# Optimization experiments

Hardware: AMD Instinct MI355X
Metric: run time of the kernel (lower is better)

Reference implementation:

```python
import jax, jax.numpy as jnp
import numpy as np

M = 5            # players per side
N = 100000       # nodes (players)
E = 1000000      # edges (matches)
W = 7 * M        # hidden width (width_RP hard-coded to 7 in __init__)
D = 3            # depth_RP hard-coded to 3
NORM_FACTOR = 2.0


def _linear_params(k, out_d, in_d):
    bound = 1.0 / np.sqrt(in_d)
    kw, kb = jax.random.split(k)
    w = jax.random.uniform(kw, (out_d, in_d), jnp.float32, -bound, bound)
    b = jax.random.uniform(kb, (out_d,), jnp.float32, -bound, bound)
    return w, b


def setup_inputs() -> dict:
    key = jax.random.key(0)
    ks = jax.random.split(key, 12)
    score = jax.random.normal(ks[0], (N, 1), jnp.float32)
    edge_idx = jax.random.randint(ks[1], (E, 2 * M), 0, N, dtype=jnp.int32)
    outcome = 2.0 * jax.random.randint(ks[2], (E,), 0, 2).astype(jnp.float32) - 1.0  # in {-1,+1}

    R_start_w, R_start_b = _linear_params(ks[3], W, 2 * M)
    rh = [_linear_params(k, W, W) for k in jax.random.split(ks[4], D)]
    R_hid_w = jnp.stack([w for w, _ in rh]); R_hid_b = jnp.stack([b for _, b in rh])
    R_end_w, R_end_b = _linear_params(ks[5], 2 * M, W)

    P_start_w, P_start_b = _linear_params(ks[6], W, 2 * M)
    ph = [_linear_params(k, W, W) for k in jax.random.split(ks[7], D)]
    P_hid_w = jnp.stack([w for w, _ in ph]); P_hid_b = jnp.stack([b for _, b in ph])
    P_end_w, P_end_b = _linear_params(ks[8], 2 * M, W)

    return dict(score=score, edge_idx=edge_idx, outcome=outcome,
                R_start_w=R_start_w, R_start_b=R_start_b, R_hid_w=R_hid_w, R_hid_b=R_hid_b,
                R_end_w=R_end_w, R_end_b=R_end_b,
                P_start_w=P_start_w, P_start_b=P_start_b, P_hid_w=P_hid_w, P_hid_b=P_hid_b,
                P_end_w=P_end_w, P_end_b=P_end_b)


def _mlp(x, sw, sb, hw, hb, ew, eb):
    h = jax.nn.relu(x @ sw.T + sb)
    for i in range(D):
        h = jax.nn.relu(h @ hw[i].T + hb[i])
    return h @ ew.T + eb


def reference(score, edge_idx, outcome,
              R_start_w, R_start_b, R_hid_w, R_hid_b, R_end_w, R_end_b,
              P_start_w, P_start_b, P_hid_w, P_hid_b, P_end_w, P_end_b):
    # gather per-edge node scores: [E, 2M]
    node_score = score[edge_idx, 0]
    node_score_rev = node_score[:, ::-1]

    reward = _mlp(node_score, R_start_w, R_start_b, R_hid_w, R_hid_b, R_end_w, R_end_b)
    penalty = _mlp(node_score, P_start_w, P_start_b, P_hid_w, P_hid_b, P_end_w, P_end_b)
    reward_rev = _mlp(node_score_rev, R_start_w, R_start_b, R_hid_w, R_hid_b, R_end_w, R_end_b)
    penalty_rev = _mlp(node_score_rev, P_start_w, P_start_b, P_hid_w, P_hid_b, P_end_w, P_end_b)

    e01 = (outcome + 1.0) * 0.5  # [E] in {0,1}
    contribute = e01[:, None] * jax.nn.sigmoid(reward) - (1.0 - e01)[:, None] * jax.nn.sigmoid(penalty)
    contribute_rev = (1.0 - e01)[:, None] * jax.nn.sigmoid(reward_rev) - e01[:, None] * jax.nn.sigmoid(penalty_rev)

    # original loop only uses columns 0..M-1 of contribute (-> edge_idx[:, :M])
    # and columns 0..M-1 of contribute_rev (-> edge_idx[:, M:2M])
    vals = jnp.concatenate([contribute[:, :M], contribute_rev[:, :M]], axis=1).ravel()  # [E*2M]
    idx = edge_idx.ravel()                                                              # [E*2M]
    agg = jax.ops.segment_sum(vals, idx, num_segments=N)
    deg = jax.ops.segment_sum(jnp.ones_like(vals), idx, num_segments=N)

    agg = agg / (deg.max() / NORM_FACTOR)
    s = score + agg[:, None]
    s = s - s.mean()
    s = s / jnp.linalg.norm(s, axis=0)  # L2 norm over nodes, broadcast [1]
    return s
```

## Files before the change

### kernel.cpp

```cpp
#include <hip/hip_runtime.h>
#include <hip/hip_bf16.h>
#include <hip/hip_fp16.h>

typedef _Float16 f16x8 __attribute__((ext_vector_type(8)));
typedef float    f32x4 __attribute__((ext_vector_type(4)));

#define NNODES 100000
#define NEDGES 1000000

#define PK_SCALE   1048576.0
#define PK_INV     9.5367431640625e-07

#define WS_AGGD   0u
#define WS_STATS  800000u
#define WS_DEGMAX 800008u
#define WS_CNTS   800012u
#define WS_ZERO_BYTES 800020u
#define WS_FRAGS  800032u
#define WS_LIST   906528u

#define NTILES_PER_NET 26

__global__ void __launch_bounds__(64) prep_frag_kernel(
    const float* __restrict__ Rsw, const float* __restrict__ Rsb,
    const float* __restrict__ Rhw, const float* __restrict__ Rhb,
    const float* __restrict__ Rew, const float* __restrict__ Reb,
    const float* __restrict__ Psw, const float* __restrict__ Psb,
    const float* __restrict__ Phw, const float* __restrict__ Phb,
    const float* __restrict__ Pew, const float* __restrict__ Peb,
    unsigned short* __restrict__ frags)
{
    const int t = blockIdx.x;
    const int l = threadIdx.x;
    const int net = t / NTILES_PER_NET;
    const int tt  = t % NTILES_PER_NET;
    const float *sw, *sb, *hw, *hb, *ew, *eb;
    if (net == 0) { sw=Rsw; sb=Rsb; hw=Rhw; hb=Rhb; ew=Rew; eb=Reb; }
    else          { sw=Psw; sb=Psb; hw=Phw; hb=Phb; ew=Pew; eb=Peb; }

    int layer, mt, kt = 0, rev = 0;
    if (tt < 6)       { layer = 0; rev = (tt >= 3); mt = tt % 3; }
    else if (tt < 24) { int u = tt - 6; layer = 1 + u / 6; u %= 6; mt = u / 2; kt = u % 2; }
    else              { layer = 4; mt = 0; kt = tt - 24; }

    const int m     = mt * 16 + (l & 15);
    const int kbase = kt * 32 + (l >> 4) * 8;

    unsigned short hi8[8], lo8[8];
    #pragma unroll
    for (int j = 0; j < 8; ++j) {
        const int k = kbase + j;
        float v = 0.0f;
        if (layer == 0) {
            if (m < 35) { if (k < 10) v = sw[m * 10 + (rev ? 9 - k : k)];
                          else if (k == 10) v = sb[m]; }
        } else if (layer <= 3) {
            if (m < 35) { if (k < 35) v = hw[(layer - 1) * 1225 + m * 35 + k];
                          else if (k == 35) v = hb[(layer - 1) * 35 + m]; }
        } else {
            if (m < 5)  { if (k < 35) v = ew[m * 35 + k];
                          else if (k == 35) v = eb[m]; }
        }
        _Float16 h = (_Float16)v;
        _Float16 lo = (_Float16)(v - (float)h);
        hi8[j] = __builtin_bit_cast(unsigned short, h);
        lo8[j] = __builtin_bit_cast(unsigned short, lo);
    }
    unsigned short* bh = frags + ((size_t)(t * 2 + 0) * 64 + l) * 8;
    unsigned short* bl = frags + ((size_t)(t * 2 + 1) * 64 + l) * 8;
    #pragma unroll
    for (int j = 0; j < 8; ++j) { bh[j] = hi8[j]; bl[j] = lo8[j]; }
}

__global__ void __launch_bounds__(256) sort_kernel(
    const float* __restrict__ outcome, int* __restrict__ list, int* __restrict__ cnts)
{
    __shared__ int wTotP[4], wTotN[4], wBaseP[4], wBaseN[4], blkP, blkN;
    const int tid = threadIdx.x, wv = tid >> 6, lane = tid & 63;

    #pragma unroll 1
    for (int start = blockIdx.x * 2048; start < NEDGES; start += gridDim.x * 2048) {
        const int e0 = start + tid * 8;
        int valid[8], isp[8];
        int pc = 0, nc = 0;
        #pragma unroll
        for (int j = 0; j < 8; ++j) {
            const int e = e0 + j;
            valid[j] = (e < NEDGES);
            float o = valid[j] ? outcome[e] : 0.0f;
            isp[j] = valid[j] && (o > 0.0f);
            pc += isp[j];
            nc += (valid[j] && !isp[j]);
        }
        int pi = pc, ni = nc;
        #pragma unroll
        for (int off = 1; off < 64; off <<= 1) {
            int tp = __shfl_up(pi, off);
            int tn = __shfl_up(ni, off);
            if (lane >= off) { pi += tp; ni += tn; }
        }
        const int pex = pi - pc, nex = ni - nc;
        if (lane == 63) { wTotP[wv] = pi; wTotN[wv] = ni; }
        __syncthreads();
        if (tid == 0) {
            int tp = 0, tn = 0;
            #pragma unroll
            for (int w = 0; w < 4; ++w) {
                wBaseP[w] = tp; wBaseN[w] = tn;
                tp += wTotP[w]; tn += wTotN[w];
            }
            blkP = atomicAdd(&cnts[0], tp);
            blkN = atomicAdd(&cnts[1], tn);
        }
        __syncthreads();
        int pbase = blkP + wBaseP[wv] + pex;
        int nbase = blkN + wBaseN[wv] + nex;
        #pragma unroll
        for (int j = 0; j < 8; ++j) {
            if (isp[j])        list[pbase++] = e0 + j;
            else if (valid[j]) list[NEDGES - 1 - (nbase++)] = e0 + j;
        }
        __syncthreads();
    }
}

__device__ __forceinline__ unsigned int pk16(_Float16 a, _Float16 b) {
    return (unsigned int)__builtin_bit_cast(unsigned short, a) |
           ((unsigned int)__builtin_bit_cast(unsigned short, b) << 16);
}

__device__ __forceinline__ void trans_store(unsigned int* hb, int n, int rb, int mt, f32x4 v)
{
    _Float16 h0 = (_Float16)v[0], h1 = (_Float16)v[1], h2 = (_Float16)v[2], h3 = (_Float16)v[3];
    float r0 = v[0] - (float)h0, r1 = v[1] - (float)h1, r2 = v[2] - (float)h2, r3 = v[3] - (float)h3;
    unsigned int hd0 = pk16(h0, h1), hd1 = pk16(h2, h3);
    unsigned int ld0 = pk16((_Float16)r0, (_Float16)r1), ld1 = pk16((_Float16)r2, (_Float16)r3);
    const int b  = 2 * mt + (rb >> 1);
    const int bp = b ^ (n & 7);
    const int dw = n * 32 + (bp << 2) + ((rb & 1) << 1);
    *reinterpret_cast<uint2*>(hb + dw)       = make_uint2(hd0, hd1);
    *reinterpret_cast<uint2*>(hb + 512 + dw) = make_uint2(ld0, ld1);
}

__device__ __forceinline__ f16x8 read_b(const unsigned int* hb, int n, int kb, int kt, int lobuf)
{
    const int b  = kt * 4 + kb;
    const int bp = b ^ (n & 7);
    uint4 d = *reinterpret_cast<const uint4*>(hb + lobuf * 512 + n * 32 + (bp << 2));
    return __builtin_bit_cast(f16x8, d);
}

#define MF(acc, WH, WL, BH, BL)                                                    \
    acc = __builtin_amdgcn_mfma_f32_16x16x32_f16(WH, BH, acc, 0, 0, 0);            \
    acc = __builtin_amdgcn_mfma_f32_16x16x32_f16(WH, BL, acc, 0, 0, 0);            \
    acc = __builtin_amdgcn_mfma_f32_16x16x32_f16(WL, BH, acc, 0, 0, 0);

#define TRANSITION(X0, X1, X2)                                                     \
    {                                                                              \
        _Pragma("unroll")                                                          \
        for (int r = 0; r < 4; ++r) {                                              \
            X0[r] = fmaxf(X0[r], 0.0f);                                            \
            X1[r] = fmaxf(X1[r], 0.0f);                                            \
            X2[r] = fmaxf(X2[r], 0.0f);                                            \
        }                                                                          \
        if (kb == 0) X2[3] = 1.0f;                                                 \
        trans_store(hb, n, kb, 0, X0);                                             \
        trans_store(hb, n, kb, 1, X1);                                             \
        trans_store(hb, n, kb, 2, X2);                                             \
    }

#define HLAYER(U0, C0, C1, C2)                                                     \
    {                                                                              \
        f16x8 bh0 = read_b(hb, n, kb, 0, 0), bl0 = read_b(hb, n, kb, 0, 1);        \
        f16x8 bh1 = read_b(hb, n, kb, 1, 0), bl1 = read_b(hb, n, kb, 1, 1);        \
        C0 = z4; C1 = z4; C2 = z4;                                                 \
        __builtin_amdgcn_s_setprio(1);                                             \
        MF(C0, wh[(U0) + 0], wl[(U0) + 0], bh0, bl0)                               \
        MF(C0, wh[(U0) + 1], wl[(U0) + 1], bh1, bl1)                               \
        MF(C1, wh[(U0) + 2], wl[(U0) + 2], bh0, bl0)                               \
        MF(C1, wh[(U0) + 3], wl[(U0) + 3], bh1, bl1)                               \
        MF(C2, wh[(U0) + 4], wl[(U0) + 4], bh0, bl0)                               \
        MF(C2, wh[(U0) + 5], wl[(U0) + 5], bh1, bl1)                               \
        __builtin_amdgcn_s_setprio(0);                                             \
    }

__global__ void __launch_bounds__(256, 2) edge_kernel(
    const float* __restrict__ score,
    const int*   __restrict__ edge_idx,
    const unsigned short* __restrict__ frags,
    const int*   __restrict__ list,
    const int*   __restrict__ cnts,
    double* __restrict__ aggd)
{
    __shared__ unsigned int hbuf[4][1024];
    const int tid  = threadIdx.x;
    const int wv   = tid >> 6;
    const int lane = tid & 63;
    const int n    = lane & 15;
    const int kb   = lane >> 4;
    const int k0   = kb * 8;
    unsigned int* hb = &hbuf[wv][0];

    for (int i = lane; i < 1024; i += 64) hb[i] = 0;

    const int gw    = blockIdx.x * 4 + wv;
    const int combo = gw & 3;
    const int wci   = gw >> 2;

    const int cp   = cnts[0];
    const int useR = (combo < 2);
    const int rev  = (combo == 1 || combo == 2);
    const float sgn = useR ? 1.0f : -1.0f;
    const int lo_  = (combo == 0 || combo == 2) ? 0 : cp;
    const int hi_  = (combo == 0 || combo == 2) ? cp : NEDGES;
    const int cnt  = hi_ - lo_;
    const int revoff = rev ? 5 : 0;
    const int t0   = useR ? 0 : NTILES_PER_NET;

    f16x8 wh[18], wl[18];
    #pragma unroll
    for (int u = 0; u < 18; ++u) {
        const int t = t0 + 6 + u;
        wh[u] = *reinterpret_cast<const f16x8*>(frags + ((size_t)(t * 2 + 0) * 64 + lane) * 8);
        wl[u] = *reinterpret_cast<const f16x8*>(frags + ((size_t)(t * 2 + 1) * 64 + lane) * 8);
    }
    f16x8 w0h[3], w0l[3], w4h[2], w4l[2];
    #pragma unroll
    for (int mt = 0; mt < 3; ++mt) {
        const int t = t0 + (rev ? 3 : 0) + mt;
        w0h[mt] = *reinterpret_cast<const f16x8*>(frags + ((size_t)(t * 2 + 0) * 64 + lane) * 8);
        w0l[mt] = *reinterpret_cast<const f16x8*>(frags + ((size_t)(t * 2 + 1) * 64 + lane) * 8);
    }
    #pragma unroll
    for (int kt = 0; kt < 2; ++kt) {
        const int t = t0 + 24 + kt;
        w4h[kt] = *reinterpret_cast<const f16x8*>(frags + ((size_t)(t * 2 + 0) * 64 + lane) * 8);
        w4l[kt] = *reinterpret_cast<const f16x8*>(frags + ((size_t)(t * 2 + 1) * 64 + lane) * 8);
    }

    const f32x4 z4 = {0.0f, 0.0f, 0.0f, 0.0f};

    auto GATHER = [&](int b, float (&s)[8], int& edo, bool& ao) {
        ao  = (b + n) < cnt;
        edo = list[ao ? (lo_ + b + n) : lo_];
        #pragma unroll
        for (int j = 0; j < 8; ++j) {
            const int k = k0 + j;
            const int id = (k < 10) ? edge_idx[edo * 10 + k] : 0;
            s[j] = (k < 10) ? score[id] : 0.0f;
        }
        if (kb == 1) s[2] = 1.0f;
    };

    int   base = wci * 16;
    float sc[8];
    int   ecur = 0;
    bool  act  = false;
    if (base < cnt) GATHER(base, sc, ecur, act);

    #pragma unroll 1
    for (; base < cnt; ) {
        const int nbase = base + (int)gridDim.x * 16;
        float scn[8];
        int   enx  = 0;
        bool  actn = false;
        if (nbase < cnt) GATHER(nbase, scn, enx, actn);

        f16x8 bxh, bxl;
        #pragma unroll
        for (int j = 0; j < 8; ++j) {
            _Float16 h = (_Float16)sc[j];
            bxh[j] = h;
            bxl[j] = (_Float16)(sc[j] - (float)h);
        }

        f32x4 a0 = z4, a1 = z4, a2 = z4;
        __builtin_amdgcn_s_setprio(1);
        MF(a0, w0h[0], w0l[0], bxh, bxl)
        MF(a1, w0h[1], w0l[1], bxh, bxl)
        MF(a2, w0h[2], w0l[2], bxh, bxl)
        __builtin_amdgcn_s_setprio(0);
        TRANSITION(a0, a1, a2)

        f32x4 c0, c1, c2;
        HLAYER(0, c0, c1, c2)
        TRANSITION(c0, c1, c2)
        HLAYER(6, c0, c1, c2)
        TRANSITION(c0, c1, c2)
        HLAYER(12, c0, c1, c2)
        TRANSITION(c0, c1, c2)

        f32x4 c4 = z4;
        {
            f16x8 bh0 = read_b(hb, n, kb, 0, 0), bl0 = read_b(hb, n, kb, 0, 1);
            f16x8 bh1 = read_b(hb, n, kb, 1, 0), bl1 = read_b(hb, n, kb, 1, 1);
            __builtin_amdgcn_s_setprio(1);
            MF(c4, w4h[0], w4l[0], bh0, bl0)
            MF(c4, w4h[1], w4l[1], bh1, bl1)
            __builtin_amdgcn_s_setprio(0);
        }

        #pragma unroll
        for (int r = 0; r < 4; ++r) {
            const int q = kb * 4 + r;
            if (act && q < 5) {
                const float v = sgn / (1.0f + __expf(-c4[r]));
                const int tgt = edge_idx[ecur * 10 + revoff + q];
                unsafeAtomicAdd(&aggd[tgt], (double)v + PK_SCALE);
            }
        }

        base = nbase;
        #pragma unroll
        for (int j = 0; j < 8; ++j) sc[j] = scn[j];
        ecur = enx;
        act  = actn;
    }
}

__global__ void __launch_bounds__(256) degmax_kernel(const double* __restrict__ aggd,
                                                     int* __restrict__ degmax)
{
    int m = 0;
    for (int i = blockIdx.x * blockDim.x + threadIdx.x; i < NNODES;
         i += gridDim.x * blockDim.x)
        m = max(m, (int)(aggd[i] * PK_INV + 0.5));
    #pragma unroll
    for (int off = 32; off; off >>= 1) m = max(m, __shfl_down(m, off));
    __shared__ int sm[4];
    if ((threadIdx.x & 63) == 0) sm[threadIdx.x >> 6] = m;
    __syncthreads();
    if (threadIdx.x == 0) {
        int mm = sm[0];
        #pragma unroll
        for (int w = 1; w < 4; ++w) mm = max(mm, sm[w]);
        atomicMax(degmax, mm);
    }
}

__global__ void __launch_bounds__(256) stats_kernel(const float* __restrict__ score,
                                                    const double* __restrict__ aggd,
                                                    const int* __restrict__ degmax,
                                                    float* __restrict__ stats)
{
    const float scale = 2.0f / (float)(*degmax);
    float s = 0.0f, s2 = 0.0f;
    for (int i = blockIdx.x * blockDim.x + threadIdx.x; i < NNODES;
         i += gridDim.x * blockDim.x) {
        const double T = aggd[i];
        const int d = (int)(T * PK_INV + 0.5);
        const float vs = (float)(T - (double)d * PK_SCALE);
        float v = fmaf(vs, scale, score[i]);
        s += v;
        s2 = fmaf(v, v, s2);
    }
    #pragma unroll
    for (int off = 32; off; off >>= 1) {
        s  += __shfl_down(s, off);
        s2 += __shfl_down(s2, off);
    }
    __shared__ float ssum[4], ssq[4];
    if ((threadIdx.x & 63) == 0) { ssum[threadIdx.x >> 6] = s; ssq[threadIdx.x >> 6] = s2; }
    __syncthreads();
    if (threadIdx.x == 0) {
        float a = 0.0f, b = 0.0f;
        #pragma unroll
        for (int w = 0; w < 4; ++w) { a += ssum[w]; b += ssq[w]; }
        unsafeAtomicAdd(&stats[0], a);
        unsafeAtomicAdd(&stats[1], b);
    }
}

__global__ void __launch_bounds__(256) finalize_kernel(const float* __restrict__ score,
                                                       const double* __restrict__ aggd,
                                                       const int* __restrict__ degmax,
                                                       const float* __restrict__ stats,
                                                       float* __restrict__ out)
{
    const float scale = 2.0f / (float)(*degmax);
    const float sum = stats[0], sumsq = stats[1];
    const float mean = sum * (1.0f / NNODES);
    const float rn = 1.0f / sqrtf(sumsq - sum * mean);
    for (int i = blockIdx.x * blockDim.x + threadIdx.x; i < NNODES;
         i += gridDim.x * blockDim.x) {
        const double T = aggd[i];
        const int d = (int)(T * PK_INV + 0.5);
        const float vs = (float)(T - (double)d * PK_SCALE);
        float v = fmaf(vs, scale, score[i]);
        out[i] = (v - mean) * rn;
    }
}

extern "C" void kernel_launch(void* const* d_in, const int* in_sizes, int n_in,
                              void* d_out, int out_size, void* d_ws, size_t ws_size,
                              hipStream_t stream)
{
    const float* score    = (const float*)d_in[0];
    const int*   edge_idx = (const int*)  d_in[1];
    const float* outcome  = (const float*)d_in[2];
    const float* Rsw = (const float*)d_in[3];
    const float* Rsb = (const float*)d_in[4];
    const float* Rhw = (const float*)d_in[5];
    const float* Rhb = (const float*)d_in[6];
    const float* Rew = (const float*)d_in[7];
    const float* Reb = (const float*)d_in[8];
    const float* Psw = (const float*)d_in[9];
    const float* Psb = (const float*)d_in[10];
    const float* Phw = (const float*)d_in[11];
    const float* Phb = (const float*)d_in[12];
    const float* Pew = (const float*)d_in[13];
    const float* Peb = (const float*)d_in[14];
    float* out = (float*)d_out;

    char* ws = (char*)d_ws;
    double*         aggd   = (double*)(ws + WS_AGGD);
    float*          stats  = (float*)(ws + WS_STATS);
    int*            degmax = (int*)  (ws + WS_DEGMAX);
    int*            cnts   = (int*)  (ws + WS_CNTS);
    unsigned short* frags  = (unsigned short*)(ws + WS_FRAGS);
    int*            list   = (int*)  (ws + WS_LIST);

    hipMemsetAsync(d_ws, 0, WS_ZERO_BYTES, stream);

    prep_frag_kernel<<<52, 64, 0, stream>>>(Rsw, Rsb, Rhw, Rhb, Rew, Reb,
                                            Psw, Psb, Phw, Phb, Pew, Peb, frags);
    sort_kernel<<<256, 256, 0, stream>>>(outcome, list, cnts);

    edge_kernel<<<2048, 256, 0, stream>>>(score, edge_idx, frags, list, cnts, aggd);

    const int nb = (NNODES + 255) / 256;
    degmax_kernel  <<<nb, 256, 0, stream>>>(aggd, degmax);
    stats_kernel   <<<nb, 256, 0, stream>>>(score, aggd, degmax, stats);
    finalize_kernel<<<nb, 256, 0, stream>>>(score, aggd, degmax, stats, out);
}
```

Measured before the change: 662.5 us.

## Replace global double atomics with record emission plus bucket sort and shared-memory reduction

The edge kernel can now write (target, value) records to a 10M-entry buffer instead of doing global fp64 atomics. A histogram, column scan, scatter and per-bucket shared-memory fixed-point reduction then compute per-node sums and degrees. This path runs only when the workspace holds about 169 MB, otherwise the old atomic path is used. It trades contended global atomics for roughly 160 MB of extra record traffic and several extra kernel launches.

```diff
diff --git a/kernel.cpp b/kernel.cpp
--- a/kernel.cpp
+++ b/kernel.cpp
@@ -7,17 +7,29 @@
 
 #define NNODES 100000
 #define NEDGES 1000000
+#define NREC   10000000ll
 
 #define PK_SCALE   1048576.0
 #define PK_INV     9.5367431640625e-07
 
-#define WS_AGGD   0u
+#define WS_AGG    0u
+#define WS_DEG    400000u
 #define WS_STATS  800000u
 #define WS_DEGMAX 800008u
 #define WS_CNTS   800012u
-#define WS_ZERO_BYTES 800020u
+#define WS_ZERO_END 800020u
 #define WS_FRAGS  800032u
 #define WS_LIST   906528u
+#define WS_BASE   4906528u
+#define WS_COLT   4907584u
+#define WS_HIST   4908608u
+#define WS_OFFS   7005760u
+#define WS_RECS   9102912u
+#define WS_BINN   89102912u
+#define WS_NEED   169102912u
+
+#define S3_BLOCKS 2048
+#define S3_CHUNK  4883ll
 
 #define NTILES_PER_NET 26
 
@@ -184,13 +196,15 @@
         __builtin_amdgcn_s_setprio(0);                                             \
     }
 
+template<int MODE>
 __global__ void __launch_bounds__(256, 2) edge_kernel(
     const float* __restrict__ score,
     const int*   __restrict__ edge_idx,
     const unsigned short* __restrict__ frags,
     const int*   __restrict__ list,
     const int*   __restrict__ cnts,
-    double* __restrict__ aggd)
+    double* __restrict__ aggd,
+    unsigned long long* __restrict__ recs)
 {
     __shared__ unsigned int hbuf[4][1024];
     const int tid  = threadIdx.x;
@@ -306,7 +320,14 @@
             if (act && q < 5) {
                 const float v = sgn / (1.0f + __expf(-c4[r]));
                 const int tgt = edge_idx[ecur * 10 + revoff + q];
-                unsafeAtomicAdd(&aggd[tgt], (double)v + PK_SCALE);
+                if (MODE == 0) {
+                    unsafeAtomicAdd(&aggd[tgt], (double)v + PK_SCALE);
+                } else {
+                    const unsigned long long rcd =
+                        ((unsigned long long)(unsigned)tgt << 32) |
+                        (unsigned long long)__float_as_uint(v);
+                    recs[(long long)(lo_ + base + n) * 10 + revoff + q] = rcd;
+                }
             }
         }
 
@@ -318,13 +339,118 @@
     }
 }
 
-__global__ void __launch_bounds__(256) degmax_kernel(const double* __restrict__ aggd,
+
+__global__ void __launch_bounds__(256) hist_kernel(const unsigned long long* __restrict__ recs,
+                                                   unsigned* __restrict__ hist)
+{
+    __shared__ unsigned h[256];
+    const int t = threadIdx.x;
+    h[t] = 0;
+    __syncthreads();
+    const long long lo = (long long)blockIdx.x * S3_CHUNK;
+    const long long hi = (lo + S3_CHUNK < NREC) ? lo + S3_CHUNK : NREC;
+    for (long long i = lo + t; i < hi; i += 256)
+        atomicAdd(&h[(unsigned)(recs[i] >> 41)], 1u);
+    __syncthreads();
+    hist[blockIdx.x * 256 + t] = h[t];
+}
+
+__global__ void __launch_bounds__(256) colscan_kernel(const unsigned* __restrict__ hist,
+                                                      unsigned* __restrict__ offs,
+                                                      unsigned* __restrict__ colT)
+{
+    const int b = blockIdx.x;
+    const int t = threadIdx.x, lane = t & 63, wv = t >> 6;
+    unsigned v[8]; unsigned s = 0;
+    #pragma unroll
+    for (int j = 0; j < 8; ++j) { v[j] = hist[(t * 8 + j) * 256 + b]; s += v[j]; }
+    unsigned si = s;
+    #pragma unroll
+    for (int off = 1; off < 64; off <<= 1) {
+        unsigned tv = __shfl_up(si, off);
+        if (lane >= off) si += tv;
+    }
+    __shared__ unsigned wt[4], wb[4];
+    if (lane == 63) wt[wv] = si;
+    __syncthreads();
+    if (t == 0) {
+        unsigned a = 0;
+        #pragma unroll
+        for (int w = 0; w < 4; ++w) { wb[w] = a; a += wt[w]; }
+        colT[b] = a;
+    }
+    __syncthreads();
+    unsigned basee = wb[wv] + (si - s);
+    #pragma unroll
+    for (int j = 0; j < 8; ++j) { offs[(t * 8 + j) * 256 + b] = basee; basee += v[j]; }
+}
+
+__global__ void basescan_kernel(const unsigned* __restrict__ colT, unsigned* __restrict__ base)
+{
+    if (threadIdx.x == 0) {
+        unsigned a = 0;
+        for (int b = 0; b < 256; ++b) { base[b] = a; a += colT[b]; }
+        base[256] = a;
+    }
+}
+
+__global__ void __launch_bounds__(256) scatter_kernel(const unsigned long long* __restrict__ recs,
+                                                      const unsigned* __restrict__ offs,
+                                                      const unsigned* __restrict__ base,
+                                                      unsigned long long* __restrict__ binned)
+{
+    __shared__ unsigned cur[256];
+    const int t = threadIdx.x;
+    cur[t] = offs[blockIdx.x * 256 + t] + base[t];
+    __syncthreads();
+    const long long lo = (long long)blockIdx.x * S3_CHUNK;
+    const long long hi = (lo + S3_CHUNK < NREC) ? lo + S3_CHUNK : NREC;
+    for (long long i = lo + t; i < hi; i += 256) {
+        const unsigned long long r = recs[i];
+        const unsigned p = atomicAdd(&cur[(unsigned)(r >> 41)], 1u);
+        binned[p] = r;
+    }
+}
+
+__global__ void __launch_bounds__(256) reduce_kernel(const unsigned long long* __restrict__ binned,
+                                                     const unsigned* __restrict__ base,
+                                                     float* __restrict__ agg,
+                                                     int* __restrict__ deg)
+{
+    __shared__ unsigned long long bins[512];
+    const int t = threadIdx.x;
+    bins[t] = 0; bins[t + 256] = 0;
+    __syncthreads();
+    const int b = blockIdx.x;
+    const unsigned lo = base[b], hi = base[b + 1];
+    for (unsigned i = lo + t; i < hi; i += 256) {
+        const unsigned long long r = binned[i];
+        const int local = (int)((r >> 32) & 511);
+        const float v = __uint_as_float((unsigned)r);
+        const long long c = (long long)llrintf(v * 4294967296.0f) + (1ll << 44);
+        atomicAdd(&bins[local], (unsigned long long)c);
+    }
+    __syncthreads();
+    #pragma unroll
+    for (int j = 0; j < 2; ++j) {
+        const int local = t + j * 256;
+        const int node = b * 512 + local;
+        if (node < NNODES) {
+            const unsigned long long T = bins[local];
+            const long long d = (long long)((T + (1ll << 43)) >> 44);
+            const long long S = (long long)(T - ((unsigned long long)d << 44));
+            agg[node] = (float)((double)S * (1.0 / 4294967296.0));
+            deg[node] = (int)d;
+        }
+    }
+}
+
+__global__ void __launch_bounds__(256) degmax_kernel(const int* __restrict__ deg,
                                                      int* __restrict__ degmax)
 {
     int m = 0;
-    for (int i = blockIdx.x * blockDim.x + threadIdx.x; i < NNODES;
-         i += gridDim.x * blockDim.x)
-        m = max(m, (int)(aggd[i] * PK_INV + 0.5));
+    for (int i = blockIdx.x * blockDim.x + threadIdx.x; i < NNODES; i += gridDim.x * blockDim.x)
+        m = max(m, deg[i]);
     #pragma unroll
     for (int off = 32; off; off >>= 1) m = max(m, __shfl_down(m, off));
     __shared__ int sm[4];
@@ -339,14 +465,74 @@
 }
 
 __global__ void __launch_bounds__(256) stats_kernel(const float* __restrict__ score,
-                                                    const double* __restrict__ aggd,
+                                                    const float* __restrict__ agg,
                                                     const int* __restrict__ degmax,
                                                     float* __restrict__ stats)
 {
     const float scale = 2.0f / (float)(*degmax);
     float s = 0.0f, s2 = 0.0f;
-    for (int i = blockIdx.x * blockDim.x + threadIdx.x; i < NNODES;
-         i += gridDim.x * blockDim.x) {
+    for (int i = blockIdx.x * blockDim.x + threadIdx.x; i < NNODES; i += gridDim.x * blockDim.x) {
+        float v = fmaf(agg[i], scale, score[i]);
+        s += v;
+        s2 = fmaf(v, v, s2);
+    }
+    #pragma unroll
+    for (int off = 32; off; off >>= 1) { s += __shfl_down(s, off); s2 += __shfl_down(s2, off); }
+    __shared__ float ssum[4], ssq[4];
+    if ((threadIdx.x & 63) == 0) { ssum[threadIdx.x >> 6] = s; ssq[threadIdx.x >> 6] = s2; }
+    __syncthreads();
+    if (threadIdx.x == 0) {
+        float a = 0.0f, b = 0.0f;
+        #pragma unroll
+        for (int w = 0; w < 4; ++w) { a += ssum[w]; b += ssq[w]; }
+        unsafeAtomicAdd(&stats[0], a);
+        unsafeAtomicAdd(&stats[1], b);
+    }
+}
+
+__global__ void __launch_bounds__(256) finalize_kernel(const float* __restrict__ score,
+                                                       const float* __restrict__ agg,
+                                                       const int* __restrict__ degmax,
+                                                       const float* __restrict__ stats,
+                                                       float* __restrict__ out)
+{
+    const float scale = 2.0f / (float)(*degmax);
+    const float sum = stats[0], sumsq = stats[1];
+    const float mean = sum * (1.0f / NNODES);
+    const float rn = 1.0f / sqrtf(sumsq - sum * mean);
+    for (int i = blockIdx.x * blockDim.x + threadIdx.x; i < NNODES; i += gridDim.x * blockDim.x) {
+        float v = fmaf(agg[i], scale, score[i]);
+        out[i] = (v - mean) * rn;
+    }
+}
+
+__global__ void __launch_bounds__(256) degmax_pk(const double* __restrict__ aggd,
+                                                 int* __restrict__ degmax)
+{
+    int m = 0;
+    for (int i = blockIdx.x * blockDim.x + threadIdx.x; i < NNODES; i += gridDim.x * blockDim.x)
+        m = max(m, (int)(aggd[i] * PK_INV + 0.5));
+    #pragma unroll
+    for (int off = 32; off; off >>= 1) m = max(m, __shfl_down(m, off));
+    __shared__ int sm[4];
+    if ((threadIdx.x & 63) == 0) sm[threadIdx.x >> 6] = m;
+    __syncthreads();
+    if (threadIdx.x == 0) {
+        int mm = sm[0];
+        #pragma unroll
+        for (int w = 1; w < 4; ++w) mm = max(mm, sm[w]);
+        atomicMax(degmax, mm);
+    }
+}
+
+__global__ void __launch_bounds__(256) stats_pk(const float* __restrict__ score,
+                                                const double* __restrict__ aggd,
+                                                const int* __restrict__ degmax,
+                                                float* __restrict__ stats)
+{
+    const float scale = 2.0f / (float)(*degmax);
+    float s = 0.0f, s2 = 0.0f;
+    for (int i = blockIdx.x * blockDim.x + threadIdx.x; i < NNODES; i += gridDim.x * blockDim.x) {
         const double T = aggd[i];
         const int d = (int)(T * PK_INV + 0.5);
         const float vs = (float)(T - (double)d * PK_SCALE);
@@ -355,10 +541,7 @@
         s2 = fmaf(v, v, s2);
     }
     #pragma unroll
-    for (int off = 32; off; off >>= 1) {
-        s  += __shfl_down(s, off);
-        s2 += __shfl_down(s2, off);
-    }
+    for (int off = 32; off; off >>= 1) { s += __shfl_down(s, off); s2 += __shfl_down(s2, off); }
     __shared__ float ssum[4], ssq[4];
     if ((threadIdx.x & 63) == 0) { ssum[threadIdx.x >> 6] = s; ssq[threadIdx.x >> 6] = s2; }
     __syncthreads();
@@ -371,18 +554,17 @@
     }
 }
 
-__global__ void __launch_bounds__(256) finalize_kernel(const float* __restrict__ score,
-                                                       const double* __restrict__ aggd,
-                                                       const int* __restrict__ degmax,
-                                                       const float* __restrict__ stats,
-                                                       float* __restrict__ out)
+__global__ void __launch_bounds__(256) finalize_pk(const float* __restrict__ score,
+                                                   const double* __restrict__ aggd,
+                                                   const int* __restrict__ degmax,
+                                                   const float* __restrict__ stats,
+                                                   float* __restrict__ out)
 {
     const float scale = 2.0f / (float)(*degmax);
     const float sum = stats[0], sumsq = stats[1];
     const float mean = sum * (1.0f / NNODES);
     const float rn = 1.0f / sqrtf(sumsq - sum * mean);
-    for (int i = blockIdx.x * blockDim.x + threadIdx.x; i < NNODES;
-         i += gridDim.x * blockDim.x) {
+    for (int i = blockIdx.x * blockDim.x + threadIdx.x; i < NNODES; i += gridDim.x * blockDim.x) {
         const double T = aggd[i];
         const int d = (int)(T * PK_INV + 0.5);
         const float vs = (float)(T - (double)d * PK_SCALE);
@@ -413,23 +595,45 @@
     float* out = (float*)d_out;
 
     char* ws = (char*)d_ws;
-    double*         aggd   = (double*)(ws + WS_AGGD);
-    float*          stats  = (float*)(ws + WS_STATS);
-    int*            degmax = (int*)  (ws + WS_DEGMAX);
-    int*            cnts   = (int*)  (ws + WS_CNTS);
-    unsigned short* frags  = (unsigned short*)(ws + WS_FRAGS);
-    int*            list   = (int*)  (ws + WS_LIST);
-
-    hipMemsetAsync(d_ws, 0, WS_ZERO_BYTES, stream);
+    float*              agg    = (float*)(ws + WS_AGG);
+    int*                deg    = (int*)  (ws + WS_DEG);
+    double*             aggd   = (double*)(ws + WS_AGG);
+    float*              stats  = (float*)(ws + WS_STATS);
+    int*                degmax = (int*)  (ws + WS_DEGMAX);
+    int*                cnts   = (int*)  (ws + WS_CNTS);
+    unsigned short*     frags  = (unsigned short*)(ws + WS_FRAGS);
+    int*                list   = (int*)  (ws + WS_LIST);
+    unsigned*           basep  = (unsigned*)(ws + WS_BASE);
+    unsigned*           colT   = (unsigned*)(ws + WS_COLT);
+    unsigned*           hist   = (unsigned*)(ws + WS_HIST);
+    unsigned*           offs   = (unsigned*)(ws + WS_OFFS);
+    unsigned long long* recs   = (unsigned long long*)(ws + WS_RECS);
+    unsigned long long* binned = (unsigned long long*)(ws + WS_BINN);
+
+    const bool fast = (ws_size >= (size_t)WS_NEED);
+    const int nb = (NNODES + 255) / 256;
 
     prep_frag_kernel<<<52, 64, 0, stream>>>(Rsw, Rsb, Rhw, Rhb, Rew, Reb,
                                             Psw, Psb, Phw, Phb, Pew, Peb, frags);
-    sort_kernel<<<256, 256, 0, stream>>>(outcome, list, cnts);
-
-    edge_kernel<<<2048, 256, 0, stream>>>(score, edge_idx, frags, list, cnts, aggd);
-
-    const int nb = (NNODES + 255) / 256;
-    degmax_kernel  <<<nb, 256, 0, stream>>>(aggd, degmax);
-    stats_kernel   <<<nb, 256, 0, stream>>>(score, aggd, degmax, stats);
-    finalize_kernel<<<nb, 256, 0, stream>>>(score, aggd, degmax, stats, out);
-}
+
+    if (fast) {
+        hipMemsetAsync(ws + WS_STATS, 0, WS_ZERO_END - WS_STATS, stream);
+        sort_kernel<<<256, 256, 0, stream>>>(outcome, list, cnts);
+        edge_kernel<1><<<2048, 256, 0, stream>>>(score, edge_idx, frags, list, cnts, aggd, recs);
+        hist_kernel    <<<S3_BLOCKS, 256, 0, stream>>>(recs, hist);
+        colscan_kernel <<<256, 256, 0, stream>>>(hist, offs, colT);
+        basescan_kernel<<<1, 64, 0, stream>>>(colT, basep);
+        scatter_kernel <<<S3_BLOCKS, 256, 0, stream>>>(recs, offs, basep, binned);
+        reduce_kernel  <<<196, 256, 0, stream>>>(binned, basep, agg, deg);
+        degmax_kernel  <<<nb, 256, 0, stream>>>(deg, degmax);
+        stats_kernel   <<<nb, 256, 0, stream>>>(score, agg, degmax, stats);
+        finalize_kernel<<<nb, 256, 0, stream>>>(score, agg, degmax, stats, out);
+    } else {
+        hipMemsetAsync(d_ws, 0, WS_ZERO_END, stream);
+        sort_kernel<<<256, 256, 0, stream>>>(outcome, list, cnts);
+        edge_kernel<0><<<2048, 256, 0, stream>>>(score, edge_idx, frags, list, cnts, aggd, recs);
+        degmax_pk  <<<nb, 256, 0, stream>>>(aggd, degmax);
+        stats_pk   <<<nb, 256, 0, stream>>>(score, aggd, degmax, stats);
+        finalize_pk<<<nb, 256, 0, stream>>>(score, aggd, degmax, stats, out);
+    }
+}
```

Measured after the change: 603.8 us. 1.1x faster.
